# Kernel optimization log

Measured on AMD Instinct MI355X. Metric: run time of the kernel, lower is better.

The kernel has to match this reference:

```python
import jax, jax.numpy as jnp
import numpy as np

B, C, L, M, F, N = 4, 32, 256, 256, 8, 64  # N = L // 4 per build()


def setup_inputs() -> dict:
    key = jax.random.key(0)
    k1, k2, k3, k4 = jax.random.split(key, 4)
    return {
        "x_real": jax.random.normal(k1, (B, 1, C, L, M), dtype=jnp.float32),
        "x_imag": jax.random.normal(k2, (B, 1, C, L, M), dtype=jnp.float32),
        "w_real": jax.random.normal(k3, (F, C, N, 1), dtype=jnp.float32),
        "w_imag": jax.random.normal(k4, (F, C, N, 1), dtype=jnp.float32),
    }


def _interp_weights(w, L):
    """tfp.math.interp_regular_1d_grid along axis=-2: map x_targ=0..L-1 over
    ref range [0, L-1] onto an N-point regular grid, linear interpolation."""
    Nn = w.shape[-2]
    t = jnp.arange(L, dtype=jnp.float32) / (L - 1) * (Nn - 1)  # grid coords
    lo = jnp.clip(jnp.floor(t).astype(jnp.int32), 0, Nn - 2)
    frac = (t - lo.astype(jnp.float32))[:, None]               # (L, 1)
    return w[:, :, lo, :] * (1.0 - frac) + w[:, :, lo + 1, :] * frac  # (F,C,L,1)


def reference(x_real, x_imag, w_real, w_imag):
    Lm = x_real.shape[-2]
    wr = _interp_weights(w_real, Lm)  # (F, C, L, 1)
    wi = _interp_weights(w_imag, Lm)
    # complex multiply: (wr + i*wi) * (xr + i*xi), broadcast (B,1,C,L,M)->(B,F,C,L,M)
    pr = wr * x_real - wi * x_imag
    pi = wr * x_imag + wi * x_real
    scale = jnp.sqrt(1.0 + jnp.arange(Lm, dtype=jnp.float32))[:, None]  # self.l, (L,1)
    yr = jnp.mean(pr, axis=-3) * scale  # (B, F, L, M)
    yi = jnp.mean(pi, axis=-3) * scale
    yr = jax.nn.relu(yr)  # relu=True: relu applied to real part only
    return jnp.stack([yr, yi])  # (2, B, F, L, M) == (real, imag)
```

## Files before the change

kernel.cpp:

```cpp
#include <hip/hip_runtime.h>
#include <math.h>

constexpr int B_ = 4, C_ = 32, L_ = 256, M_ = 256, F_ = 8, N_ = 64;

__global__ __launch_bounds__(256, 4) void sphereconv_kernel(
    const float* __restrict__ xr, const float* __restrict__ xi,
    const float* __restrict__ wr, const float* __restrict__ wi,
    float* __restrict__ out)
{
    __shared__ float ws[C_ * 16];
    __shared__ float red[32 * 128];

    const int b   = blockIdx.x >> 8;
    const int l   = blockIdx.x & (L_ - 1);
    const int tid = threadIdx.x;
    const int grp = tid >> 7;
    const int t   = tid & 127;

    const float tc = ((float)l / (float)(L_ - 1)) * (float)(N_ - 1);
    int lo = (int)floorf(tc);
    if (lo > N_ - 2) lo = N_ - 2;
    const float frac = tc - (float)lo;

#pragma unroll
    for (int i = tid; i < C_ * 16; i += 256) {
        const int c = i >> 4;
        const int j = i & 15;
        const int f = j & 7;
        const float* w = (j & 8) ? wi : wr;
        const int base = (f * C_ + c) * N_ + lo;
        ws[c * 16 + j] = w[base] * (1.0f - frac) + w[base + 1] * frac;
    }
    __syncthreads();

    float2 accr[F_], acci[F_];
#pragma unroll
    for (int f = 0; f < F_; ++f) {
        accr[f] = make_float2(0.f, 0.f);
        acci[f] = make_float2(0.f, 0.f);
    }

    const int c0 = grp * 16;
    const size_t strideC2 = (size_t)L_ * M_ / 2;
    const size_t xoff = ((size_t)b * C_ + c0) * L_ * M_ + (size_t)l * M_ + t * 2;
    const float2* xr2 = (const float2*)(xr + xoff);
    const float2* xi2 = (const float2*)(xi + xoff);

#define CX(f, A, Bv)                                          \
    accr[f].x = fmaf(A, vr.x, fmaf(-(Bv), vi.x, accr[f].x));  \
    accr[f].y = fmaf(A, vr.y, fmaf(-(Bv), vi.y, accr[f].y));  \
    acci[f].x = fmaf(A, vi.x, fmaf((Bv), vr.x, acci[f].x));   \
    acci[f].y = fmaf(A, vi.y, fmaf((Bv), vr.y, acci[f].y));

#pragma unroll 8
    for (int c = 0; c < 16; ++c) {
        const float2 vr = xr2[c * strideC2];
        const float2 vi = xi2[c * strideC2];
        const float* wp = &ws[(c0 + c) * 16];
        const float4 a0 = *(const float4*)(wp + 0);
        const float4 a1 = *(const float4*)(wp + 4);
        const float4 b0 = *(const float4*)(wp + 8);
        const float4 b1 = *(const float4*)(wp + 12);
        CX(0, a0.x, b0.x)
        CX(1, a0.y, b0.y)
        CX(2, a0.z, b0.z)
        CX(3, a0.w, b0.w)
        CX(4, a1.x, b1.x)
        CX(5, a1.y, b1.y)
        CX(6, a1.z, b1.z)
        CX(7, a1.w, b1.w)
    }
#undef CX

    if (grp == 1) {
#pragma unroll
        for (int f = 0; f < F_; ++f) {
            red[(f * 4 + 0) * 128 + t] = accr[f].x;
            red[(f * 4 + 1) * 128 + t] = accr[f].y;
            red[(f * 4 + 2) * 128 + t] = acci[f].x;
            red[(f * 4 + 3) * 128 + t] = acci[f].y;
        }
    }
    __syncthreads();
    if (grp == 0) {
        const float scale = sqrtf(1.0f + (float)l) * (1.0f / (float)C_);
        const size_t o0      = (((size_t)b * F_) * L_ + l) * M_ + t * 2;
        const size_t imagOff = (size_t)B_ * F_ * L_ * M_;
        const size_t fStride = (size_t)L_ * M_;
#pragma unroll
        for (int f = 0; f < F_; ++f) {
            float2 yr, yi;
            yr.x = fmaxf((accr[f].x + red[(f * 4 + 0) * 128 + t]) * scale, 0.f);
            yr.y = fmaxf((accr[f].y + red[(f * 4 + 1) * 128 + t]) * scale, 0.f);
            yi.x = (acci[f].x + red[(f * 4 + 2) * 128 + t]) * scale;
            yi.y = (acci[f].y + red[(f * 4 + 3) * 128 + t]) * scale;
            *(float2*)(out + o0 + (size_t)f * fStride)           = yr;
            *(float2*)(out + o0 + (size_t)f * fStride + imagOff) = yi;
        }
    }
}

extern "C" void kernel_launch(void* const* d_in, const int* in_sizes, int n_in,
                              void* d_out, int out_size, void* d_ws, size_t ws_size,
                              hipStream_t stream) {
    const float* xr = (const float*)d_in[0];
    const float* xi = (const float*)d_in[1];
    const float* wr = (const float*)d_in[2];
    const float* wi = (const float*)d_in[3];
    float* out = (float*)d_out;
    sphereconv_kernel<<<dim3(B_ * L_), dim3(256), 0, stream>>>(xr, xi, wr, wi, out);
}
```

Measured before the change: 107.9 us.

## Use float4 loads with 128-thread blocks and prefetch all channel inputs into registers

Each block now has 128 threads in two waves. Each lane handles four consecutive M elements through float4 loads and stores, where before each of 256 threads handled two. All 16 channel loads per lane are issued up front into registers, so many memory requests are in flight before the FMA loop starts. This aims to hide load latency on this bandwidth-bound kernel. In exchange, register pressure rises substantially (64 float4 values), which may limit occupancy or cause spills.

```diff
diff --git a/kernel.cpp b/kernel.cpp
--- a/kernel.cpp
+++ b/kernel.cpp
@@ -3,19 +3,19 @@
 
 constexpr int B_ = 4, C_ = 32, L_ = 256, M_ = 256, F_ = 8, N_ = 64;
 
-__global__ __launch_bounds__(256, 4) void sphereconv_kernel(
+__global__ __launch_bounds__(128, 2) void sphereconv_kernel(
     const float* __restrict__ xr, const float* __restrict__ xi,
     const float* __restrict__ wr, const float* __restrict__ wi,
     float* __restrict__ out)
 {
-    __shared__ float ws[C_ * 16];
-    __shared__ float red[32 * 128];
+    __shared__ float  ws[C_ * 16];
+    __shared__ float4 red[16 * 64];
 
-    const int b   = blockIdx.x >> 8;
-    const int l   = blockIdx.x & (L_ - 1);
-    const int tid = threadIdx.x;
-    const int grp = tid >> 7;
-    const int t   = tid & 127;
+    const int b    = blockIdx.x >> 8;
+    const int l    = blockIdx.x & (L_ - 1);
+    const int tid  = threadIdx.x;
+    const int wave = tid >> 6;
+    const int lane = tid & 63;
 
     const float tc = ((float)l / (float)(L_ - 1)) * (float)(N_ - 1);
     int lo = (int)floorf(tc);
@@ -23,7 +23,7 @@
     const float frac = tc - (float)lo;
 
 #pragma unroll
-    for (int i = tid; i < C_ * 16; i += 256) {
+    for (int i = tid; i < C_ * 16; i += 128) {
         const int c = i >> 4;
         const int j = i & 15;
         const int f = j & 7;
@@ -33,29 +33,40 @@
     }
     __syncthreads();
 
-    float2 accr[F_], acci[F_];
+    const int c0 = wave * 16;
+    const size_t strideC4 = (size_t)L_ * M_ / 4;
+    const size_t xoff = ((size_t)b * C_ + c0) * L_ * M_ + (size_t)l * M_ + lane * 4;
+    const float4* xr4 = (const float4*)(xr + xoff);
+    const float4* xi4 = (const float4*)(xi + xoff);
+
+    float4 xv_r[16], xv_i[16];
+#pragma unroll
+    for (int c = 0; c < 16; ++c) {
+        xv_r[c] = xr4[c * strideC4];
+        xv_i[c] = xi4[c * strideC4];
+    }
+
+    float4 accr[F_], acci[F_];
 #pragma unroll
     for (int f = 0; f < F_; ++f) {
-        accr[f] = make_float2(0.f, 0.f);
-        acci[f] = make_float2(0.f, 0.f);
+        accr[f] = make_float4(0.f, 0.f, 0.f, 0.f);
+        acci[f] = make_float4(0.f, 0.f, 0.f, 0.f);
     }
-
-    const int c0 = grp * 16;
-    const size_t strideC2 = (size_t)L_ * M_ / 2;
-    const size_t xoff = ((size_t)b * C_ + c0) * L_ * M_ + (size_t)l * M_ + t * 2;
-    const float2* xr2 = (const float2*)(xr + xoff);
-    const float2* xi2 = (const float2*)(xi + xoff);
 
 #define CX(f, A, Bv)                                          \
     accr[f].x = fmaf(A, vr.x, fmaf(-(Bv), vi.x, accr[f].x));  \
     accr[f].y = fmaf(A, vr.y, fmaf(-(Bv), vi.y, accr[f].y));  \
+    accr[f].z = fmaf(A, vr.z, fmaf(-(Bv), vi.z, accr[f].z));  \
+    accr[f].w = fmaf(A, vr.w, fmaf(-(Bv), vi.w, accr[f].w));  \
     acci[f].x = fmaf(A, vi.x, fmaf((Bv), vr.x, acci[f].x));   \
-    acci[f].y = fmaf(A, vi.y, fmaf((Bv), vr.y, acci[f].y));
+    acci[f].y = fmaf(A, vi.y, fmaf((Bv), vr.y, acci[f].y));   \
+    acci[f].z = fmaf(A, vi.z, fmaf((Bv), vr.z, acci[f].z));   \
+    acci[f].w = fmaf(A, vi.w, fmaf((Bv), vr.w, acci[f].w));
 
-#pragma unroll 8
+#pragma unroll
     for (int c = 0; c < 16; ++c) {
-        const float2 vr = xr2[c * strideC2];
-        const float2 vi = xi2[c * strideC2];
+        const float4 vr = xv_r[c];
+        const float4 vi = xv_i[c];
         const float* wp = &ws[(c0 + c) * 16];
         const float4 a0 = *(const float4*)(wp + 0);
         const float4 a1 = *(const float4*)(wp + 4);
@@ -72,30 +83,34 @@
     }
 #undef CX
 
-    if (grp == 1) {
+    if (wave == 1) {
 #pragma unroll
         for (int f = 0; f < F_; ++f) {
-            red[(f * 4 + 0) * 128 + t] = accr[f].x;
-            red[(f * 4 + 1) * 128 + t] = accr[f].y;
-            red[(f * 4 + 2) * 128 + t] = acci[f].x;
-            red[(f * 4 + 3) * 128 + t] = acci[f].y;
+            red[(f * 2 + 0) * 64 + lane] = accr[f];
+            red[(f * 2 + 1) * 64 + lane] = acci[f];
         }
     }
     __syncthreads();
-    if (grp == 0) {
+    if (wave == 0) {
         const float scale = sqrtf(1.0f + (float)l) * (1.0f / (float)C_);
-        const size_t o0      = (((size_t)b * F_) * L_ + l) * M_ + t * 2;
+        const size_t o0      = (((size_t)b * F_) * L_ + l) * M_ + lane * 4;
         const size_t imagOff = (size_t)B_ * F_ * L_ * M_;
         const size_t fStride = (size_t)L_ * M_;
 #pragma unroll
         for (int f = 0; f < F_; ++f) {
-            float2 yr, yi;
-            yr.x = fmaxf((accr[f].x + red[(f * 4 + 0) * 128 + t]) * scale, 0.f);
-            yr.y = fmaxf((accr[f].y + red[(f * 4 + 1) * 128 + t]) * scale, 0.f);
-            yi.x = (acci[f].x + red[(f * 4 + 2) * 128 + t]) * scale;
-            yi.y = (acci[f].y + red[(f * 4 + 3) * 128 + t]) * scale;
-            *(float2*)(out + o0 + (size_t)f * fStride)           = yr;
-            *(float2*)(out + o0 + (size_t)f * fStride + imagOff) = yi;
+            const float4 pr = red[(f * 2 + 0) * 64 + lane];
+            const float4 pi = red[(f * 2 + 1) * 64 + lane];
+            float4 yr, yi;
+            yr.x = fmaxf((accr[f].x + pr.x) * scale, 0.f);
+            yr.y = fmaxf((accr[f].y + pr.y) * scale, 0.f);
+            yr.z = fmaxf((accr[f].z + pr.z) * scale, 0.f);
+            yr.w = fmaxf((accr[f].w + pr.w) * scale, 0.f);
+            yi.x = (acci[f].x + pi.x) * scale;
+            yi.y = (acci[f].y + pi.y) * scale;
+            yi.z = (acci[f].z + pi.z) * scale;
+            yi.w = (acci[f].w + pi.w) * scale;
+            *(float4*)(out + o0 + (size_t)f * fStride)           = yr;
+            *(float4*)(out + o0 + (size_t)f * fStride + imagOff) = yi;
         }
     }
 }
@@ -108,5 +123,5 @@
     const float* wr = (const float*)d_in[2];
     const float* wi = (const float*)d_in[3];
     float* out = (float*)d_out;
-    sphereconv_kernel<<<dim3(B_ * L_), dim3(256), 0, stream>>>(xr, xi, wr, wi, out);
+    sphereconv_kernel<<<dim3(B_ * L_), dim3(128), 0, stream>>>(xr, xi, wr, wi, out);
 }
```

Result: no change. 107.8 us (-0.1%).
